# Kernel optimization log

Measured on AMD Instinct MI355X. Metric: run time of the kernel, lower is better.

## Reference

```python
import jax, jax.numpy as jnp
import numpy as np

N_NODES = 100000
N_EDGES = 1600000
IN_CH = 128
TYPE_EMB = 32
OUT_CH = 128
N_REL = 8
N_BASES = 8
N_NTYPES = 8
FEAT = IN_CH + TYPE_EMB  # 160, RGCNConv input dim after concat


def setup_inputs() -> dict:
    key = jax.random.key(0)
    ks = jax.random.split(key, 9)
    x = jax.random.normal(ks[0], (N_NODES, IN_CH), dtype=jnp.float32)
    node_type_ids = jax.random.randint(ks[1], (N_NODES,), 0, N_NTYPES)
    edge_index = jax.random.randint(ks[2], (2, N_EDGES), 0, N_NODES)
    edge_type = jax.random.randint(ks[3], (N_EDGES,), 0, N_REL)
    emb_table = jax.random.normal(ks[4], (N_NTYPES, TYPE_EMB), dtype=jnp.float32)
    bases = jax.random.normal(ks[5], (N_BASES, FEAT, OUT_CH), dtype=jnp.float32) * (1.0 / np.sqrt(FEAT))
    comp = jax.random.normal(ks[6], (N_REL, N_BASES), dtype=jnp.float32) * (1.0 / np.sqrt(N_BASES))
    root_w = jax.random.normal(ks[7], (FEAT, OUT_CH), dtype=jnp.float32) * (1.0 / np.sqrt(FEAT))
    bias = jnp.zeros((OUT_CH,), dtype=jnp.float32)
    return {"x": x, "node_type_ids": node_type_ids, "edge_index": edge_index,
            "edge_type": edge_type, "emb_table": emb_table, "bases": bases,
            "comp": comp, "root_w": root_w, "bias": bias}


def reference(x, node_type_ids, edge_index, edge_type, emb_table, bases, comp, root_w, bias):
    N = x.shape[0]
    # node-type embedding lookup + concat
    h = jnp.concatenate([x, emb_table[node_type_ids]], axis=1)  # [N, FEAT]
    # basis decomposition: per-relation weights [R, FEAT, OUT]
    weight = jnp.einsum('rb,bio->rio', comp, bases)
    src, dst = edge_index[0], edge_index[1]
    h_src = h[src]  # [E, FEAT] -- dominant gather
    # root/self transform + bias
    out = h @ root_w + bias
    # PyG RGCNConv default aggr='mean': per-relation mean over incoming edges, summed across relations
    for r in range(weight.shape[0]):
        m = (edge_type == r).astype(h.dtype)  # [E]
        s = jax.ops.segment_sum(h_src * m[:, None], dst, num_segments=N)  # [N, FEAT]
        c = jax.ops.segment_sum(m, dst, num_segments=N)                    # [N]
        mean_r = s / jnp.maximum(c, 1.0)[:, None]
        out = out + mean_r @ weight[r]
    # dropout is identity in eval mode
    return jax.nn.relu(out)
```

## Files before the change

### kernel.cpp

```cpp
#include <hip/hip_runtime.h>

#define NN 100000
#define NE 1600000
#define INC 128
#define TE 32
#define OC 128
#define NR 8
#define NBASES 8
#define FT 160
#define KP 168
#define KW 160
#define TN 32
#define NBKT 3125
#define NCH 128
#define EPB 12500
#define CAP 896

typedef float f32x4 __attribute__((ext_vector_type(4)));
typedef float f32x2 __attribute__((ext_vector_type(2)));
typedef __bf16 bf16x8 __attribute__((ext_vector_type(8)));

__device__ __forceinline__ unsigned f2bf1(float f) {
    unsigned u = __float_as_uint(f);
    return (u + 0x7fffu + ((u >> 16) & 1u)) >> 16;
}

__device__ __forceinline__ float bflo(unsigned u) { return __uint_as_float(u << 16); }
__device__ __forceinline__ float bfhi(unsigned u) { return __uint_as_float(u & 0xFFFF0000u); }

__device__ __forceinline__ unsigned cvtpk(float a, float b) {
    unsigned r;
    asm("v_cvt_pk_bf16_f32 %0, %1, %2" : "=v"(r) : "v"(a), "v"(b));
    return r;
}

__device__ __forceinline__ int bscan_excl(int v, int* tmp) {
    int tid = threadIdx.x;
    tmp[tid] = v; __syncthreads();
#pragma unroll
    for (int d = 1; d < 256; d <<= 1) {
        int t = (tid >= d) ? tmp[tid - d] : 0;
        __syncthreads();
        tmp[tid] += t;
        __syncthreads();
    }
    return tmp[tid] - v;
}

__global__ __launch_bounds__(256) void k_prep(
    const float* __restrict__ x, const int* __restrict__ nt,
    const float* __restrict__ emb, const float* __restrict__ comp,
    const float* __restrict__ bases, const float* __restrict__ rootw,
    const int* __restrict__ ei,
    unsigned short* __restrict__ h, unsigned short* __restrict__ Wt,
    int* __restrict__ ghist, int* __restrict__ total) {
    __shared__ int hist[NBKT];
    int tid = threadIdx.x;
    int b = blockIdx.x;
    if (b < NCH) {
        for (int j = tid; j < NBKT; j += 256) hist[j] = 0;
        __syncthreads();
        int e0 = b * EPB;
#pragma unroll
        for (int k = 0; k < 49; k++) {
            int i = k * 256 + tid;
            if (i < EPB) atomicAdd(&hist[ei[NE + e0 + i] >> 5], 1);
        }
        __syncthreads();
        int* g = ghist + (size_t)b * NBKT;
        for (int j = tid; j < NBKT; j += 256) {
            int v = hist[j];
            g[j] = v;
            if (v) atomicAdd(&total[j], v);
        }
        return;
    }
    int idx = (b - NCH) * 256 + tid;
    if (idx < 9 * 128 * KW) {
        int ridx = idx / (128 * KW);
        int rem  = idx % (128 * KW);
        int o = rem / KW;
        int k = rem % KW;
        float v;
        if (ridx < NR) {
            v = 0.f;
#pragma unroll
            for (int bb = 0; bb < NBASES; bb++)
                v += comp[ridx * NBASES + bb] * bases[(bb * FT + k) * OC + o];
        } else {
            v = rootw[k * OC + o];
        }
        Wt[idx] = (unsigned short)f2bf1(v);
    }
    if (idx < NN * 20) {
        int n = idx / 20, c = idx % 20;
        f32x4 v0, v1;
        if (c < 16) {
            const float* p = x + (size_t)n * INC + c * 8;
            v0 = *(const f32x4*)p; v1 = *(const f32x4*)(p + 4);
        } else {
            int tt = nt[n];
            const float* p = emb + tt * TE + (c - 16) * 8;
            v0 = *(const f32x4*)p; v1 = *(const f32x4*)(p + 4);
        }
        uint4 o;
        o.x = f2bf1(v0.x) | (f2bf1(v0.y) << 16);
        o.y = f2bf1(v0.z) | (f2bf1(v0.w) << 16);
        o.z = f2bf1(v1.x) | (f2bf1(v1.y) << 16);
        o.w = f2bf1(v1.z) | (f2bf1(v1.w) << 16);
        *(uint4*)(h + (size_t)n * FT + c * 8) = o;
    }
}

__global__ __launch_bounds__(256) void k_scanoff(const int* __restrict__ total,
                                                 int* __restrict__ ghist,
                                                 int* __restrict__ bstart) {
    __shared__ int tot[NBKT];
    __shared__ int tmp[256];
    int tid = threadIdx.x;
    for (int j = tid; j < NBKT; j += 256) tot[j] = total[j];
    __syncthreads();
    int i0 = tid * 13, s = 0;
    int loc[13];
#pragma unroll
    for (int i = 0; i < 13; i++) {
        int j = i0 + i;
        loc[i] = (j < NBKT) ? tot[j] : 0;
        s += loc[i];
    }
    int run = bscan_excl(s, tmp);
#pragma unroll
    for (int i = 0; i < 13; i++) {
        int j = i0 + i;
        if (j < NBKT) tot[j] = run;
        run += loc[i];
    }
    __syncthreads();
    if (blockIdx.x == 0) {
        for (int j = tid; j < NBKT; j += 256) bstart[j] = tot[j];
        if (tid == 0) bstart[NBKT] = NE;
    }
    int j = blockIdx.x * 256 + tid;
    if (j < NBKT) {
        int run2 = tot[j];
#pragma unroll 4
        for (int b = 0; b < NCH; b++) {
            int v = ghist[(size_t)b * NBKT + j];
            ghist[(size_t)b * NBKT + j] = run2;
            run2 += v;
        }
    }
}

__global__ __launch_bounds__(256) void k_scatter(const int* __restrict__ ei, const int* __restrict__ et,
                                                 const int* __restrict__ ghist, unsigned* __restrict__ slots) {
    __shared__ int cur[NBKT];
    int tid = threadIdx.x, b = blockIdx.x;
    for (int j = tid; j < NBKT; j += 256) cur[j] = ghist[(size_t)b * NBKT + j];
    __syncthreads();
    int e0 = b * EPB;
#pragma unroll
    for (int k = 0; k < 49; k++) {
        int i = k * 256 + tid;
        if (i < EPB) {
            int e = e0 + i;
            int s = ei[e], d = ei[NE + e], r = et[e];
            int pos = atomicAdd(&cur[d >> 5], 1);
            slots[pos] = (unsigned)s | ((unsigned)r << 17) | ((unsigned)(d & 31) << 20);
        }
    }
}

__global__ __launch_bounds__(256, 6) void k_mega(
    const unsigned short* __restrict__ h, const float* __restrict__ bias,
    const unsigned short* __restrict__ Wt, const int* __restrict__ bstart,
    const unsigned* __restrict__ slots, float* __restrict__ out) {
    __shared__ unsigned short featmem[2][TN * KP];
    __shared__ unsigned sl[CAP];
    __shared__ unsigned pkl[256];

    const int tid = threadIdx.x;
    const int lane = tid & 63;
    const int wave = tid >> 6;
    const int j = blockIdx.x;
    const int n0 = j * TN;

    unsigned* sl_in = reinterpret_cast<unsigned*>(&featmem[0][0]);
    int* hist = reinterpret_cast<int*>(&featmem[0][0]) + CAP;
    int* tmp  = reinterpret_cast<int*>(&featmem[0][0]) + CAP + 256;

    int s0 = bstart[j];
    int m = bstart[j + 1] - s0; if (m > CAP) m = CAP;
    for (int i = tid; i < m; i += 256) sl_in[i] = slots[s0 + i];
    hist[tid] = 0;
    __syncthreads();
    for (int i = tid; i < m; i += 256) {
        unsigned v = sl_in[i];
        atomicAdd(&hist[((v >> 17) & 7u) * 32u + ((v >> 20) & 31u)], 1);
    }
    __syncthreads();
    int v0 = hist[tid];
    int ex = bscan_excl(v0, tmp);
    pkl[tid] = (unsigned)ex | ((unsigned)v0 << 16);
    hist[tid] = ex;
    __syncthreads();
    for (int i = tid; i < m; i += 256) {
        unsigned v = sl_in[i];
        int p = atomicAdd(&hist[((v >> 17) & 7u) * 32u + ((v >> 20) & 31u)], 1);
        sl[p] = v & 0x1FFFFu;
    }
    __syncthreads();

    for (int i = tid; i < TN * 20; i += 256) {
        int nl = i / 20, c = i % 20, n = n0 + nl;
        uint4 v = *reinterpret_cast<const uint4*>(h + (size_t)n * FT + c * 8);
        *reinterpret_cast<uint4*>(&featmem[0][nl * KP + c * 8]) = v;
    }

    f32x4 acc[4];
#pragma unroll
    for (int t = 0; t < 4; t++) acc[t] = (f32x4){0.f, 0.f, 0.f, 0.f};

    auto mfma_pass = [&](int ridx, const unsigned short* fm) {
        const unsigned short* fA = fm + (lane & 15) * KP + ((lane >> 4) * 8);
        const unsigned short* gB = Wt + (size_t)ridx * 128 * KW
                                   + (wave * 32 + (lane & 15)) * KW + ((lane >> 4) * 8);
#pragma unroll
        for (int kc = 0; kc < 5; kc++) {
            bf16x8 a0 = *reinterpret_cast<const bf16x8*>(fA + 0 * 16 * KP + kc * 32);
            bf16x8 a1 = *reinterpret_cast<const bf16x8*>(fA + 1 * 16 * KP + kc * 32);
#pragma unroll
            for (int ct = 0; ct < 2; ct++) {
                bf16x8 b = *reinterpret_cast<const bf16x8*>(gB + ct * 16 * KW + kc * 32);
                acc[0 * 2 + ct] = __builtin_amdgcn_mfma_f32_16x16x32_bf16(a0, b, acc[0 * 2 + ct], 0, 0, 0);
                acc[1 * 2 + ct] = __builtin_amdgcn_mfma_f32_16x16x32_bf16(a1, b, acc[1 * 2 + ct], 0, 0, 0);
            }
        }
    };

    const int g = tid >> 4, l = tid & 15;
    const unsigned* hw = reinterpret_cast<const unsigned*>(h);

    auto agg_pass = [&](int r, unsigned short* fm) {
        int b0 = r * 32 + 2 * g;
        unsigned pk0 = pkl[b0], pk1 = pkl[b0 + 1];
        int sbeg = (int)(pk0 & 0xffffu);
        int e1 = (int)(pk1 & 0xffffu);
        int send = e1 + (int)(pk1 >> 16);
        f32x2 sa[5];
#pragma unroll
        for (int i = 0; i < 5; i++) sa[i] = (f32x2){0.f, 0.f};
        float run = 0.f;
        for (int e = sbeg; e < send; e += 4) {
            uint4 wv[4]; unsigned tv[4];
#pragma unroll
            for (int u = 0; u < 4; u++) {
                int eu = e + u; if (eu >= send) eu = send - 1;
                const unsigned* hp = hw + (size_t)sl[eu] * 80;
                wv[u] = *reinterpret_cast<const uint4*>(hp + 4 * l);
                tv[u] = hp[64 + l];
            }
#pragma unroll
            for (int u = 0; u < 4; u++) {
                if (e + u < send) {
                    sa[0] += (f32x2){bflo(wv[u].x), bfhi(wv[u].x)};
                    sa[1] += (f32x2){bflo(wv[u].y), bfhi(wv[u].y)};
                    sa[2] += (f32x2){bflo(wv[u].z), bfhi(wv[u].z)};
                    sa[3] += (f32x2){bflo(wv[u].w), bfhi(wv[u].w)};
                    sa[4] += (f32x2){bflo(tv[u]), bfhi(tv[u])};
                    run += 1.f;
                    int nx = e + u + 1;
                    if (nx == e1 || nx == send) {
                        int q = (e + u >= e1) ? 1 : 0;
                        float inv = __builtin_amdgcn_rcpf(run);
                        f32x2 m0 = sa[0] * inv, m1 = sa[1] * inv, m2 = sa[2] * inv,
                              m3 = sa[3] * inv, m4 = sa[4] * inv;
                        unsigned* fp = reinterpret_cast<unsigned*>(fm + (2 * g + q) * KP);
                        uint4 o;
                        o.x = cvtpk(m0.x, m0.y);
                        o.y = cvtpk(m1.x, m1.y);
                        o.z = cvtpk(m2.x, m2.y);
                        o.w = cvtpk(m3.x, m3.y);
                        *reinterpret_cast<uint4*>(fp + 4 * l) = o;
                        fp[64 + l] = cvtpk(m4.x, m4.y);
#pragma unroll
                        for (int i = 0; i < 5; i++) sa[i] = (f32x2){0.f, 0.f};
                        run = 0.f;
                    }
                }
            }
        }
#pragma unroll
        for (int q = 0; q < 2; q++) {
            if ((pkl[b0 + q] >> 16) == 0u) {
                unsigned* fp = reinterpret_cast<unsigned*>(fm + (2 * g + q) * KP);
                *reinterpret_cast<uint4*>(fp + 4 * l) = (uint4){0u, 0u, 0u, 0u};
                fp[64 + l] = 0u;
            }
        }
    };

    __syncthreads();
    int prev = 8;
    for (int r = 0; r < NR; r++) {
        agg_pass(r, &featmem[(r + 1) & 1][0]);
        mfma_pass(prev, &featmem[r & 1][0]);
        prev = r;
        __syncthreads();
    }
    mfma_pass(7, &featmem[0][0]);

    const int rq = lane >> 4;
#pragma unroll
    for (int ct = 0; ct < 2; ct++) {
        int col = wave * 32 + ct * 16 + (lane & 15);
        float bv = bias[col];
#pragma unroll
        for (int rt = 0; rt < 2; rt++) {
#pragma unroll
            for (int i = 0; i < 4; i++) {
                int n = n0 + rt * 16 + rq * 4 + i;
                float v = acc[rt * 2 + ct][i] + bv;
                out[(size_t)n * OC + col] = v > 0.f ? v : 0.f;
            }
        }
    }
}

extern "C" void kernel_launch(void* const* d_in, const int* in_sizes, int n_in,
                              void* d_out, int out_size, void* d_ws, size_t ws_size,
                              hipStream_t stream) {
    const float* x     = (const float*)d_in[0];
    const int*   ntype = (const int*)d_in[1];
    const int*   ei    = (const int*)d_in[2];
    const int*   et    = (const int*)d_in[3];
    const float* emb   = (const float*)d_in[4];
    const float* bases = (const float*)d_in[5];
    const float* comp  = (const float*)d_in[6];
    const float* rootw = (const float*)d_in[7];
    const float* bias  = (const float*)d_in[8];
    float* out = (float*)d_out;

    char* ws = (char*)d_ws;
    unsigned short* Wt     = (unsigned short*)(ws);
    unsigned short* h      = (unsigned short*)(ws + 368640);
    int*            ghist  = (int*)(ws + 32368640);
    int*            total  = (int*)(ws + 33968640);
    int*            bstart = (int*)(ws + 33981184);
    unsigned*       slots  = (unsigned*)(ws + 33993728);

    hipMemsetAsync(total, 0, (NBKT + 1) * sizeof(int), stream);
    k_prep   <<<NCH + 7813, 256, 0, stream>>>(x, ntype, emb, comp, bases, rootw, ei, h, Wt, ghist, total);
    k_scanoff<<<13,   256, 0, stream>>>(total, ghist, bstart);
    k_scatter<<<NCH,  256, 0, stream>>>(ei, et, ghist, slots);
    k_mega   <<<NBKT, 256, 0, stream>>>(h, bias, Wt, bstart, slots, out);
}
```

Measured before the change: 350.3 us.

## Use 64-node buckets with per-wave 16-row tiles and full output width

Doubles the bucket size to 64 destination nodes and gives each wave its own 16-node feature tile. Each wave now computes all 128 output columns for its rows, so the block-wide barriers and double buffering between the aggregation and MFMA passes go away. The histogram and scatter kernels run on more chunks and batch four loads ahead of the atomics. Each wave now holds 8 accumulators and reads every weight tile, which raises register and L2 pressure. The CAP limit of 1536 edges per bucket could truncate edges in unusually dense buckets.

After: 453.8 us. +29.5%, slower.

```diff
diff --git a/kernel.cpp b/kernel.cpp
--- a/kernel.cpp
+++ b/kernel.cpp
@@ -10,11 +10,11 @@
 #define FT 160
 #define KP 168
 #define KW 160
-#define TN 32
-#define NBKT 3125
-#define NCH 128
-#define EPB 12500
-#define CAP 896
+#define TN 64
+#define NBKT 1563
+#define NCH 256
+#define EPB 6250
+#define CAP 1536
 
 typedef float f32x4 __attribute__((ext_vector_type(4)));
 typedef float f32x2 __attribute__((ext_vector_type(2)));
@@ -62,9 +62,16 @@
         __syncthreads();
         int e0 = b * EPB;
 #pragma unroll
-        for (int k = 0; k < 49; k++) {
-            int i = k * 256 + tid;
-            if (i < EPB) atomicAdd(&hist[ei[NE + e0 + i] >> 5], 1);
+        for (int kk = 0; kk < 28; kk += 4) {
+            int dv[4];
+#pragma unroll
+            for (int u = 0; u < 4; u++) {
+                int i = (kk + u) * 256 + tid;
+                dv[u] = (i < EPB) ? ei[NE + e0 + i] : -1;
+            }
+#pragma unroll
+            for (int u = 0; u < 4; u++)
+                if (dv[u] >= 0) atomicAdd(&hist[dv[u] >> 6], 1);
         }
         __syncthreads();
         int* g = ghist + (size_t)b * NBKT;
@@ -120,17 +127,17 @@
     int tid = threadIdx.x;
     for (int j = tid; j < NBKT; j += 256) tot[j] = total[j];
     __syncthreads();
-    int i0 = tid * 13, s = 0;
-    int loc[13];
-#pragma unroll
-    for (int i = 0; i < 13; i++) {
+    int i0 = tid * 7, s = 0;
+    int loc[7];
+#pragma unroll
+    for (int i = 0; i < 7; i++) {
         int j = i0 + i;
         loc[i] = (j < NBKT) ? tot[j] : 0;
         s += loc[i];
     }
     int run = bscan_excl(s, tmp);
 #pragma unroll
-    for (int i = 0; i < 13; i++) {
+    for (int i = 0; i < 7; i++) {
         int j = i0 + i;
         if (j < NBKT) tot[j] = run;
         run += loc[i];
@@ -143,7 +150,7 @@
     int j = blockIdx.x * 256 + tid;
     if (j < NBKT) {
         int run2 = tot[j];
-#pragma unroll 4
+#pragma unroll 8
         for (int b = 0; b < NCH; b++) {
             int v = ghist[(size_t)b * NBKT + j];
             ghist[(size_t)b * NBKT + j] = run2;
@@ -160,24 +167,32 @@
     __syncthreads();
     int e0 = b * EPB;
 #pragma unroll
-    for (int k = 0; k < 49; k++) {
-        int i = k * 256 + tid;
-        if (i < EPB) {
-            int e = e0 + i;
-            int s = ei[e], d = ei[NE + e], r = et[e];
-            int pos = atomicAdd(&cur[d >> 5], 1);
-            slots[pos] = (unsigned)s | ((unsigned)r << 17) | ((unsigned)(d & 31) << 20);
-        }
-    }
-}
-
-__global__ __launch_bounds__(256, 6) void k_mega(
+    for (int kk = 0; kk < 28; kk += 4) {
+        int sv[4], dv[4], rv[4];
+#pragma unroll
+        for (int u = 0; u < 4; u++) {
+            int i = (kk + u) * 256 + tid;
+            int e = e0 + ((i < EPB) ? i : 0);
+            sv[u] = ei[e]; dv[u] = ei[NE + e]; rv[u] = et[e];
+            if (i >= EPB) dv[u] = -1;
+        }
+#pragma unroll
+        for (int u = 0; u < 4; u++) {
+            if (dv[u] >= 0) {
+                int pos = atomicAdd(&cur[dv[u] >> 6], 1);
+                slots[pos] = (unsigned)sv[u] | ((unsigned)rv[u] << 17) | ((unsigned)(dv[u] & 63) << 20);
+            }
+        }
+    }
+}
+
+__global__ __launch_bounds__(256, 5) void k_mega(
     const unsigned short* __restrict__ h, const float* __restrict__ bias,
     const unsigned short* __restrict__ Wt, const int* __restrict__ bstart,
     const unsigned* __restrict__ slots, float* __restrict__ out) {
-    __shared__ unsigned short featmem[2][TN * KP];
+    __shared__ unsigned short featmem[4][16 * KP];
     __shared__ unsigned sl[CAP];
-    __shared__ unsigned pkl[256];
+    __shared__ unsigned pkl[512];
 
     const int tid = threadIdx.x;
     const int lane = tid & 63;
@@ -187,66 +202,71 @@
 
     unsigned* sl_in = reinterpret_cast<unsigned*>(&featmem[0][0]);
     int* hist = reinterpret_cast<int*>(&featmem[0][0]) + CAP;
-    int* tmp  = reinterpret_cast<int*>(&featmem[0][0]) + CAP + 256;
+    int* tmp  = reinterpret_cast<int*>(&featmem[0][0]) + CAP + 512;
 
     int s0 = bstart[j];
     int m = bstart[j + 1] - s0; if (m > CAP) m = CAP;
     for (int i = tid; i < m; i += 256) sl_in[i] = slots[s0 + i];
-    hist[tid] = 0;
+    for (int k = tid; k < 512; k += 256) hist[k] = 0;
     __syncthreads();
     for (int i = tid; i < m; i += 256) {
         unsigned v = sl_in[i];
-        atomicAdd(&hist[((v >> 17) & 7u) * 32u + ((v >> 20) & 31u)], 1);
-    }
-    __syncthreads();
-    int v0 = hist[tid];
-    int ex = bscan_excl(v0, tmp);
-    pkl[tid] = (unsigned)ex | ((unsigned)v0 << 16);
-    hist[tid] = ex;
+        atomicAdd(&hist[((v >> 17) & 7u) * 64u + ((v >> 20) & 63u)], 1);
+    }
+    __syncthreads();
+    int v0 = hist[2 * tid], v1 = hist[2 * tid + 1];
+    int ex = bscan_excl(v0 + v1, tmp);
+    pkl[2 * tid]     = (unsigned)ex | ((unsigned)v0 << 16);
+    pkl[2 * tid + 1] = (unsigned)(ex + v0) | ((unsigned)v1 << 16);
+    hist[2 * tid] = ex; hist[2 * tid + 1] = ex + v0;
     __syncthreads();
     for (int i = tid; i < m; i += 256) {
         unsigned v = sl_in[i];
-        int p = atomicAdd(&hist[((v >> 17) & 7u) * 32u + ((v >> 20) & 31u)], 1);
+        int p = atomicAdd(&hist[((v >> 17) & 7u) * 64u + ((v >> 20) & 31u) + ((v >> 20) & 32u)], 1);
         sl[p] = v & 0x1FFFFu;
     }
     __syncthreads();
 
-    for (int i = tid; i < TN * 20; i += 256) {
-        int nl = i / 20, c = i % 20, n = n0 + nl;
+    unsigned short* ftile = &featmem[wave][0];
+
+    for (int i = lane; i < 16 * 20; i += 64) {
+        int nl = i / 20, c = i % 20;
+        int n = n0 + wave * 16 + nl;
         uint4 v = *reinterpret_cast<const uint4*>(h + (size_t)n * FT + c * 8);
-        *reinterpret_cast<uint4*>(&featmem[0][nl * KP + c * 8]) = v;
-    }
-
-    f32x4 acc[4];
-#pragma unroll
-    for (int t = 0; t < 4; t++) acc[t] = (f32x4){0.f, 0.f, 0.f, 0.f};
-
-    auto mfma_pass = [&](int ridx, const unsigned short* fm) {
-        const unsigned short* fA = fm + (lane & 15) * KP + ((lane >> 4) * 8);
+        *reinterpret_cast<uint4*>(&ftile[nl * KP + c * 8]) = v;
+    }
+
+    f32x4 acc[8];
+#pragma unroll
+    for (int t = 0; t < 8; t++) acc[t] = (f32x4){0.f, 0.f, 0.f, 0.f};
+
+    auto mfma_pass = [&](int ridx) {
+        const unsigned short* fA = ftile + (lane & 15) * KP + ((lane >> 4) * 8);
         const unsigned short* gB = Wt + (size_t)ridx * 128 * KW
-                                   + (wave * 32 + (lane & 15)) * KW + ((lane >> 4) * 8);
+                                   + (lane & 15) * KW + ((lane >> 4) * 8);
 #pragma unroll
         for (int kc = 0; kc < 5; kc++) {
-            bf16x8 a0 = *reinterpret_cast<const bf16x8*>(fA + 0 * 16 * KP + kc * 32);
-            bf16x8 a1 = *reinterpret_cast<const bf16x8*>(fA + 1 * 16 * KP + kc * 32);
-#pragma unroll
-            for (int ct = 0; ct < 2; ct++) {
+            bf16x8 a = *reinterpret_cast<const bf16x8*>(fA + kc * 32);
+#pragma unroll
+            for (int ct = 0; ct < 8; ct++) {
                 bf16x8 b = *reinterpret_cast<const bf16x8*>(gB + ct * 16 * KW + kc * 32);
-                acc[0 * 2 + ct] = __builtin_amdgcn_mfma_f32_16x16x32_bf16(a0, b, acc[0 * 2 + ct], 0, 0, 0);
-                acc[1 * 2 + ct] = __builtin_amdgcn_mfma_f32_16x16x32_bf16(a1, b, acc[1 * 2 + ct], 0, 0, 0);
+                acc[ct] = __builtin_amdgcn_mfma_f32_16x16x32_bf16(a, b, acc[ct], 0, 0, 0);
             }
         }
     };
 
-    const int g = tid >> 4, l = tid & 15;
+    mfma_pass(8);
+
+    const int g0 = lane >> 4, l = lane & 15;
     const unsigned* hw = reinterpret_cast<const unsigned*>(h);
-
-    auto agg_pass = [&](int r, unsigned short* fm) {
-        int b0 = r * 32 + 2 * g;
-        unsigned pk0 = pkl[b0], pk1 = pkl[b0 + 1];
-        int sbeg = (int)(pk0 & 0xffffu);
-        int e1 = (int)(pk1 & 0xffffu);
-        int send = e1 + (int)(pk1 >> 16);
+    for (int r = 0; r < NR; r++) {
+        int b0 = r * 64 + wave * 16 + 4 * g0;
+        unsigned p0 = pkl[b0], p1 = pkl[b0 + 1], p2 = pkl[b0 + 2], p3 = pkl[b0 + 3];
+        int sbeg = (int)(p0 & 0xffffu);
+        int e1 = (int)(p1 & 0xffffu);
+        int e2 = (int)(p2 & 0xffffu);
+        int e3 = (int)(p3 & 0xffffu);
+        int send = e3 + (int)(p3 >> 16);
         f32x2 sa[5];
 #pragma unroll
         for (int i = 0; i < 5; i++) sa[i] = (f32x2){0.f, 0.f};
@@ -270,12 +290,12 @@
                     sa[4] += (f32x2){bflo(tv[u]), bfhi(tv[u])};
                     run += 1.f;
                     int nx = e + u + 1;
-                    if (nx == e1 || nx == send) {
-                        int q = (e + u >= e1) ? 1 : 0;
+                    if (nx == e1 || nx == e2 || nx == e3 || nx == send) {
+                        int q = (e + u >= e1) + (e + u >= e2) + (e + u >= e3);
                         float inv = __builtin_amdgcn_rcpf(run);
                         f32x2 m0 = sa[0] * inv, m1 = sa[1] * inv, m2 = sa[2] * inv,
                               m3 = sa[3] * inv, m4 = sa[4] * inv;
-                        unsigned* fp = reinterpret_cast<unsigned*>(fm + (2 * g + q) * KP);
+                        unsigned* fp = reinterpret_cast<unsigned*>(ftile + (4 * g0 + q) * KP);
                         uint4 o;
                         o.x = cvtpk(m0.x, m0.y);
                         o.y = cvtpk(m1.x, m1.y);
@@ -291,36 +311,26 @@
             }
         }
 #pragma unroll
-        for (int q = 0; q < 2; q++) {
+        for (int q = 0; q < 4; q++) {
             if ((pkl[b0 + q] >> 16) == 0u) {
-                unsigned* fp = reinterpret_cast<unsigned*>(fm + (2 * g + q) * KP);
+                unsigned* fp = reinterpret_cast<unsigned*>(ftile + (4 * g0 + q) * KP);
                 *reinterpret_cast<uint4*>(fp + 4 * l) = (uint4){0u, 0u, 0u, 0u};
                 fp[64 + l] = 0u;
             }
         }
-    };
-
-    __syncthreads();
-    int prev = 8;
-    for (int r = 0; r < NR; r++) {
-        agg_pass(r, &featmem[(r + 1) & 1][0]);
-        mfma_pass(prev, &featmem[r & 1][0]);
-        prev = r;
-        __syncthreads();
-    }
-    mfma_pass(7, &featmem[0][0]);
+        mfma_pass(r);
+    }
 
     const int rq = lane >> 4;
 #pragma unroll
-    for (int ct = 0; ct < 2; ct++) {
-        int col = wave * 32 + ct * 16 + (lane & 15);
+    for (int ct = 0; ct < 8; ct++) {
+        int col = ct * 16 + (lane & 15);
         float bv = bias[col];
 #pragma unroll
-        for (int rt = 0; rt < 2; rt++) {
-#pragma unroll
-            for (int i = 0; i < 4; i++) {
-                int n = n0 + rt * 16 + rq * 4 + i;
-                float v = acc[rt * 2 + ct][i] + bv;
+        for (int i = 0; i < 4; i++) {
+            int n = n0 + wave * 16 + rq * 4 + i;
+            if (n < NN) {
+                float v = acc[ct][i] + bv;
                 out[(size_t)n * OC + col] = v > 0.f ? v : 0.f;
             }
         }
@@ -345,13 +355,13 @@
     unsigned short* Wt     = (unsigned short*)(ws);
     unsigned short* h      = (unsigned short*)(ws + 368640);
     int*            ghist  = (int*)(ws + 32368640);
-    int*            total  = (int*)(ws + 33968640);
-    int*            bstart = (int*)(ws + 33981184);
-    unsigned*       slots  = (unsigned*)(ws + 33993728);
+    int*            total  = (int*)(ws + 33969152);
+    int*            bstart = (int*)(ws + 33975552);
+    unsigned*       slots  = (unsigned*)(ws + 33981952);
 
     hipMemsetAsync(total, 0, (NBKT + 1) * sizeof(int), stream);
     k_prep   <<<NCH + 7813, 256, 0, stream>>>(x, ntype, emb, comp, bases, rootw, ei, h, Wt, ghist, total);
-    k_scanoff<<<13,   256, 0, stream>>>(total, ghist, bstart);
+    k_scanoff<<<7,    256, 0, stream>>>(total, ghist, bstart);
     k_scatter<<<NCH,  256, 0, stream>>>(ei, et, ghist, slots);
     k_mega   <<<NBKT, 256, 0, stream>>>(h, bias, Wt, bstart, slots, out);
 }
```

## Replace per-chunk histogram offsets with global atomic cursors; unroll gather by 8

Applied to the files above, without the earlier changes.

The bucket sort no longer stores per-chunk histograms or runs a prefix pass over them. The scan is now a single block that writes bucket starts plus a cursor array, and the scatter uses global atomics on that cursor across 1024 blocks. This removes the ghist writes and reads and the serial per-bucket loop over 128 chunks, at the cost of global atomic contention and a non-deterministic edge order within each bucket. The aggregation gather loop is also unrolled from 4 to 8 loads in flight, which raises memory-level parallelism but increases register pressure.

Result: slower. 586.3 us (+67.4%).

```diff
diff --git a/kernel.cpp b/kernel.cpp
--- a/kernel.cpp
+++ b/kernel.cpp
@@ -53,7 +53,7 @@
     const float* __restrict__ bases, const float* __restrict__ rootw,
     const int* __restrict__ ei,
     unsigned short* __restrict__ h, unsigned short* __restrict__ Wt,
-    int* __restrict__ ghist, int* __restrict__ total) {
+    int* __restrict__ total) {
     __shared__ int hist[NBKT];
     int tid = threadIdx.x;
     int b = blockIdx.x;
@@ -67,10 +67,8 @@
             if (i < EPB) atomicAdd(&hist[ei[NE + e0 + i] >> 5], 1);
         }
         __syncthreads();
-        int* g = ghist + (size_t)b * NBKT;
         for (int j = tid; j < NBKT; j += 256) {
             int v = hist[j];
-            g[j] = v;
             if (v) atomicAdd(&total[j], v);
         }
         return;
@@ -112,62 +110,34 @@
     }
 }
 
-__global__ __launch_bounds__(256) void k_scanoff(const int* __restrict__ total,
-                                                 int* __restrict__ ghist,
-                                                 int* __restrict__ bstart) {
-    __shared__ int tot[NBKT];
+__global__ __launch_bounds__(256) void k_scan(const int* __restrict__ total,
+                                              int* __restrict__ bstart,
+                                              int* __restrict__ cursor) {
     __shared__ int tmp[256];
-    int tid = threadIdx.x;
-    for (int j = tid; j < NBKT; j += 256) tot[j] = total[j];
-    __syncthreads();
-    int i0 = tid * 13, s = 0;
+    int tid = threadIdx.x, s = 0, i0 = tid * 13;
     int loc[13];
 #pragma unroll
     for (int i = 0; i < 13; i++) {
         int j = i0 + i;
-        loc[i] = (j < NBKT) ? tot[j] : 0;
+        loc[i] = (j < NBKT) ? total[j] : 0;
         s += loc[i];
     }
     int run = bscan_excl(s, tmp);
 #pragma unroll
     for (int i = 0; i < 13; i++) {
         int j = i0 + i;
-        if (j < NBKT) tot[j] = run;
-        run += loc[i];
-    }
-    __syncthreads();
-    if (blockIdx.x == 0) {
-        for (int j = tid; j < NBKT; j += 256) bstart[j] = tot[j];
-        if (tid == 0) bstart[NBKT] = NE;
-    }
-    int j = blockIdx.x * 256 + tid;
-    if (j < NBKT) {
-        int run2 = tot[j];
-#pragma unroll 4
-        for (int b = 0; b < NCH; b++) {
-            int v = ghist[(size_t)b * NBKT + j];
-            ghist[(size_t)b * NBKT + j] = run2;
-            run2 += v;
-        }
-    }
+        if (j < NBKT) { bstart[j] = run; cursor[j] = run; run += loc[i]; }
+    }
+    if (tid == 0) bstart[NBKT] = NE;
 }
 
 __global__ __launch_bounds__(256) void k_scatter(const int* __restrict__ ei, const int* __restrict__ et,
-                                                 const int* __restrict__ ghist, unsigned* __restrict__ slots) {
-    __shared__ int cur[NBKT];
-    int tid = threadIdx.x, b = blockIdx.x;
-    for (int j = tid; j < NBKT; j += 256) cur[j] = ghist[(size_t)b * NBKT + j];
-    __syncthreads();
-    int e0 = b * EPB;
-#pragma unroll
-    for (int k = 0; k < 49; k++) {
-        int i = k * 256 + tid;
-        if (i < EPB) {
-            int e = e0 + i;
-            int s = ei[e], d = ei[NE + e], r = et[e];
-            int pos = atomicAdd(&cur[d >> 5], 1);
-            slots[pos] = (unsigned)s | ((unsigned)r << 17) | ((unsigned)(d & 31) << 20);
-        }
+                                                 int* __restrict__ cursor, unsigned* __restrict__ slots) {
+    int stride = gridDim.x * 256;
+    for (int e = blockIdx.x * 256 + threadIdx.x; e < NE; e += stride) {
+        int s = ei[e], d = ei[NE + e], r = et[e];
+        int pos = atomicAdd(&cursor[d >> 5], 1);
+        slots[pos] = (unsigned)s | ((unsigned)r << 17) | ((unsigned)(d & 31) << 20);
     }
 }
 
@@ -251,17 +221,17 @@
 #pragma unroll
         for (int i = 0; i < 5; i++) sa[i] = (f32x2){0.f, 0.f};
         float run = 0.f;
-        for (int e = sbeg; e < send; e += 4) {
-            uint4 wv[4]; unsigned tv[4];
-#pragma unroll
-            for (int u = 0; u < 4; u++) {
+        for (int e = sbeg; e < send; e += 8) {
+            uint4 wv[8]; unsigned tv[8];
+#pragma unroll
+            for (int u = 0; u < 8; u++) {
                 int eu = e + u; if (eu >= send) eu = send - 1;
                 const unsigned* hp = hw + (size_t)sl[eu] * 80;
                 wv[u] = *reinterpret_cast<const uint4*>(hp + 4 * l);
                 tv[u] = hp[64 + l];
             }
 #pragma unroll
-            for (int u = 0; u < 4; u++) {
+            for (int u = 0; u < 8; u++) {
                 if (e + u < send) {
                     sa[0] += (f32x2){bflo(wv[u].x), bfhi(wv[u].x)};
                     sa[1] += (f32x2){bflo(wv[u].y), bfhi(wv[u].y)};
@@ -344,14 +314,14 @@
     char* ws = (char*)d_ws;
     unsigned short* Wt     = (unsigned short*)(ws);
     unsigned short* h      = (unsigned short*)(ws + 368640);
-    int*            ghist  = (int*)(ws + 32368640);
-    int*            total  = (int*)(ws + 33968640);
-    int*            bstart = (int*)(ws + 33981184);
-    unsigned*       slots  = (unsigned*)(ws + 33993728);
-
-    hipMemsetAsync(total, 0, (NBKT + 1) * sizeof(int), stream);
-    k_prep   <<<NCH + 7813, 256, 0, stream>>>(x, ntype, emb, comp, bases, rootw, ei, h, Wt, ghist, total);
-    k_scanoff<<<13,   256, 0, stream>>>(total, ghist, bstart);
-    k_scatter<<<NCH,  256, 0, stream>>>(ei, et, ghist, slots);
+    int*            total  = (int*)(ws + 32368640);
+    int*            bstart = (int*)(ws + 32381184);
+    int*            cursor = (int*)(ws + 32393728);
+    unsigned*       slots  = (unsigned*)(ws + 32406272);
+
+    hipMemsetAsync(total, 0, NBKT * sizeof(int), stream);
+    k_prep   <<<NCH + 7813, 256, 0, stream>>>(x, ntype, emb, comp, bases, rootw, ei, h, Wt, total);
+    k_scan   <<<1,    256, 0, stream>>>(total, bstart, cursor);
+    k_scatter<<<1024, 256, 0, stream>>>(ei, et, cursor, slots);
     k_mega   <<<NBKT, 256, 0, stream>>>(h, bias, Wt, bstart, slots, out);
 }
```

## Drop type-embedding columns from gathered features; pack source node type into edge slots

Applied to the files above, without the earlier changes.

The bf16 node feature buffer now stores only the 128 x channels per node instead of 160, so each edge gather reads 256 bytes instead of 320. The source node's type is looked up during the edge scatter and packed into the slot word. The aggregation then adds the embedding from a small shared-memory float table instead of reading it from the gathered row. This cuts gather traffic and the size of the prep pass, at the cost of an extra random nt[] read per edge in the scatter kernel. The embedding contribution is now summed in fp32 instead of from bf16-rounded values, so results can differ slightly.

New measurement: 376.3 us. 7.4% more time.

```diff
diff --git a/kernel.cpp b/kernel.cpp
--- a/kernel.cpp
+++ b/kernel.cpp
@@ -92,23 +92,16 @@
         }
         Wt[idx] = (unsigned short)f2bf1(v);
     }
-    if (idx < NN * 20) {
-        int n = idx / 20, c = idx % 20;
-        f32x4 v0, v1;
-        if (c < 16) {
-            const float* p = x + (size_t)n * INC + c * 8;
-            v0 = *(const f32x4*)p; v1 = *(const f32x4*)(p + 4);
-        } else {
-            int tt = nt[n];
-            const float* p = emb + tt * TE + (c - 16) * 8;
-            v0 = *(const f32x4*)p; v1 = *(const f32x4*)(p + 4);
-        }
+    if (idx < NN * 16) {
+        int n = idx / 16, c = idx % 16;
+        const float* p = x + (size_t)n * INC + c * 8;
+        f32x4 v0 = *(const f32x4*)p, v1 = *(const f32x4*)(p + 4);
         uint4 o;
         o.x = f2bf1(v0.x) | (f2bf1(v0.y) << 16);
         o.y = f2bf1(v0.z) | (f2bf1(v0.w) << 16);
         o.z = f2bf1(v1.x) | (f2bf1(v1.y) << 16);
         o.w = f2bf1(v1.z) | (f2bf1(v1.w) << 16);
-        *(uint4*)(h + (size_t)n * FT + c * 8) = o;
+        *(uint4*)(h + (size_t)n * INC + c * 8) = o;
     }
 }
 
@@ -153,6 +146,7 @@
 }
 
 __global__ __launch_bounds__(256) void k_scatter(const int* __restrict__ ei, const int* __restrict__ et,
+                                                 const int* __restrict__ nt,
                                                  const int* __restrict__ ghist, unsigned* __restrict__ slots) {
     __shared__ int cur[NBKT];
     int tid = threadIdx.x, b = blockIdx.x;
@@ -160,24 +154,37 @@
     __syncthreads();
     int e0 = b * EPB;
 #pragma unroll
-    for (int k = 0; k < 49; k++) {
-        int i = k * 256 + tid;
-        if (i < EPB) {
-            int e = e0 + i;
-            int s = ei[e], d = ei[NE + e], r = et[e];
-            int pos = atomicAdd(&cur[d >> 5], 1);
-            slots[pos] = (unsigned)s | ((unsigned)r << 17) | ((unsigned)(d & 31) << 20);
+    for (int kk = 0; kk < 52; kk += 4) {
+        int sv[4], dv[4], rv[4], tv[4];
+#pragma unroll
+        for (int u = 0; u < 4; u++) {
+            int i = (kk + u) * 256 + tid;
+            int e = e0 + ((i < EPB) ? i : 0);
+            sv[u] = ei[e]; dv[u] = ei[NE + e]; rv[u] = et[e];
+            if (i >= EPB) dv[u] = -1;
+        }
+#pragma unroll
+        for (int u = 0; u < 4; u++) tv[u] = nt[sv[u]];
+#pragma unroll
+        for (int u = 0; u < 4; u++) {
+            if (dv[u] >= 0) {
+                int pos = atomicAdd(&cur[dv[u] >> 5], 1);
+                slots[pos] = (unsigned)sv[u] | ((unsigned)rv[u] << 17)
+                           | ((unsigned)(dv[u] & 31) << 20) | ((unsigned)tv[u] << 25);
+            }
         }
     }
 }
 
 __global__ __launch_bounds__(256, 6) void k_mega(
-    const unsigned short* __restrict__ h, const float* __restrict__ bias,
+    const unsigned short* __restrict__ h, const int* __restrict__ nt,
+    const float* __restrict__ emb, const float* __restrict__ bias,
     const unsigned short* __restrict__ Wt, const int* __restrict__ bstart,
     const unsigned* __restrict__ slots, float* __restrict__ out) {
     __shared__ unsigned short featmem[2][TN * KP];
     __shared__ unsigned sl[CAP];
     __shared__ unsigned pkl[256];
+    __shared__ float embf[256];
 
     const int tid = threadIdx.x;
     const int lane = tid & 63;
@@ -207,13 +214,25 @@
     for (int i = tid; i < m; i += 256) {
         unsigned v = sl_in[i];
         int p = atomicAdd(&hist[((v >> 17) & 7u) * 32u + ((v >> 20) & 31u)], 1);
-        sl[p] = v & 0x1FFFFu;
-    }
-    __syncthreads();
-
+        sl[p] = (v & 0x1FFFFu) | (((v >> 25) & 7u) << 17);
+    }
+    __syncthreads();
+
+    if (tid < 256) embf[tid] = emb[tid];
     for (int i = tid; i < TN * 20; i += 256) {
         int nl = i / 20, c = i % 20, n = n0 + nl;
-        uint4 v = *reinterpret_cast<const uint4*>(h + (size_t)n * FT + c * 8);
+        uint4 v;
+        if (c < 16) {
+            v = *reinterpret_cast<const uint4*>(h + (size_t)n * INC + c * 8);
+        } else {
+            int t = nt[n];
+            const float* p = emb + t * TE + (c - 16) * 8;
+            f32x4 a = *(const f32x4*)p, bq = *(const f32x4*)(p + 4);
+            v.x = f2bf1(a.x) | (f2bf1(a.y) << 16);
+            v.y = f2bf1(a.z) | (f2bf1(a.w) << 16);
+            v.z = f2bf1(bq.x) | (f2bf1(bq.y) << 16);
+            v.w = f2bf1(bq.z) | (f2bf1(bq.w) << 16);
+        }
         *reinterpret_cast<uint4*>(&featmem[0][nl * KP + c * 8]) = v;
     }
 
@@ -252,13 +271,13 @@
         for (int i = 0; i < 5; i++) sa[i] = (f32x2){0.f, 0.f};
         float run = 0.f;
         for (int e = sbeg; e < send; e += 4) {
-            uint4 wv[4]; unsigned tv[4];
+            uint4 wv[4]; int tt[4];
 #pragma unroll
             for (int u = 0; u < 4; u++) {
                 int eu = e + u; if (eu >= send) eu = send - 1;
-                const unsigned* hp = hw + (size_t)sl[eu] * 80;
-                wv[u] = *reinterpret_cast<const uint4*>(hp + 4 * l);
-                tv[u] = hp[64 + l];
+                unsigned v = sl[eu];
+                wv[u] = *reinterpret_cast<const uint4*>(hw + (size_t)(v & 0x1FFFFu) * 64 + 4 * l);
+                tt[u] = (int)((v >> 17) & 7u);
             }
 #pragma unroll
             for (int u = 0; u < 4; u++) {
@@ -267,7 +286,7 @@
                     sa[1] += (f32x2){bflo(wv[u].y), bfhi(wv[u].y)};
                     sa[2] += (f32x2){bflo(wv[u].z), bfhi(wv[u].z)};
                     sa[3] += (f32x2){bflo(wv[u].w), bfhi(wv[u].w)};
-                    sa[4] += (f32x2){bflo(tv[u]), bfhi(tv[u])};
+                    sa[4] += *reinterpret_cast<const f32x2*>(&embf[tt[u] * 32 + 2 * l]);
                     run += 1.f;
                     int nx = e + u + 1;
                     if (nx == e1 || nx == send) {
@@ -344,14 +363,14 @@
     char* ws = (char*)d_ws;
     unsigned short* Wt     = (unsigned short*)(ws);
     unsigned short* h      = (unsigned short*)(ws + 368640);
-    int*            ghist  = (int*)(ws + 32368640);
-    int*            total  = (int*)(ws + 33968640);
-    int*            bstart = (int*)(ws + 33981184);
-    unsigned*       slots  = (unsigned*)(ws + 33993728);
-
-    hipMemsetAsync(total, 0, (NBKT + 1) * sizeof(int), stream);
-    k_prep   <<<NCH + 7813, 256, 0, stream>>>(x, ntype, emb, comp, bases, rootw, ei, h, Wt, ghist, total);
+    int*            ghist  = (int*)(ws + 25968640);
+    int*            total  = (int*)(ws + 27568640);
+    int*            bstart = (int*)(ws + 27581184);
+    unsigned*       slots  = (unsigned*)(ws + 27593728);
+
+    hipMemsetAsync(total, 0, NBKT * sizeof(int), stream);
+    k_prep   <<<NCH + 6250, 256, 0, stream>>>(x, ntype, emb, comp, bases, rootw, ei, h, Wt, ghist, total);
     k_scanoff<<<13,   256, 0, stream>>>(total, ghist, bstart);
-    k_scatter<<<NCH,  256, 0, stream>>>(ei, et, ghist, slots);
-    k_mega   <<<NBKT, 256, 0, stream>>>(h, bias, Wt, bstart, slots, out);
-}
+    k_scatter<<<NCH,  256, 0, stream>>>(ei, et, ntype, ghist, slots);
+    k_mega   <<<NBKT, 256, 0, stream>>>(h, ntype, emb, bias, Wt, bstart, slots, out);
+}
```
